# Performance work log

Measured on AMD Instinct MI355X. Metric: run time of the kernel, lower is better.

## Reference

```python
import jax, jax.numpy as jnp
import numpy as np


def setup_inputs() -> dict:
    key = jax.random.key(0)
    k1, k2, k3, k4 = jax.random.split(key, 4)
    B, D_IN, D, N, A = 32, 2048, 128, 400000, 7
    return {
        "x": jax.random.normal(k1, (B, D_IN), dtype=jnp.float32),
        "W_enc": jax.random.normal(k2, (D_IN, D), dtype=jnp.float32) * 0.02,
        "b_enc": jnp.zeros((D,), dtype=jnp.float32),
        "reps": jax.random.normal(k3, (N, D), dtype=jnp.float32),
        "actions": jax.random.normal(k4, (N, A), dtype=jnp.float32),
        "k": 5,
    }


def reference(x, W_enc, b_enc, reps, actions, k):
    # encoder embed: [B, D]
    batch_rep = x @ W_enc + b_enc
    # euclidean cdist: [B, N]
    sq = (
        jnp.sum(batch_rep * batch_rep, axis=-1, keepdims=True)
        + jnp.sum(reps * reps, axis=-1)[None, :]
        - 2.0 * (batch_rep @ reps.T)
    )
    dists = jnp.sqrt(jnp.maximum(sq, 1e-12))
    # top-k smallest distances
    neg_topk, indices = jax.lax.top_k(-dists, k)  # [B, k]
    top_k_distances = -neg_topk
    # gather actions: [B, k, A]
    top_k_actions = actions[indices]
    # softmax(-distance) weights: [B, k]
    weights = jax.nn.softmax(-top_k_distances, axis=1)
    # weighted average: [B, A]
    pred = jnp.sum(top_k_actions * weights[..., None], axis=1)
    return pred
```

## Files before the change

### kernel.cpp

```cpp
#include <hip/hip_runtime.h>
#include <math.h>

#define BATCH 32
#define DIN   2048
#define DK    128
#define NREPS 400000
#define ACT   7
#define TROWS 64
#define NTILE (NREPS / TROWS)
#define STRIDE 132
#define GDEF  694

typedef __attribute__((ext_vector_type(8))) __bf16 bf16x8;
typedef __attribute__((ext_vector_type(4))) float  f32x4;

static __device__ __forceinline__ __bf16 bits2bf(unsigned short v) {
    union { unsigned short u; __bf16 b; } x; x.u = v; return x.b;
}

__device__ __forceinline__ void topk_insert(float s, int n,
    float& d0, float& d1, float& d2, float& d3, float& d4,
    int& i0, int& i1, int& i2, int& i3, int& i4)
{
    if (s < d4) {
        if (s < d3) {
            d4 = d3; i4 = i3;
            if (s < d2) {
                d3 = d2; i3 = i2;
                if (s < d1) {
                    d2 = d1; i2 = i1;
                    if (s < d0) { d1 = d0; i1 = i0; d0 = s; i0 = n; }
                    else        { d1 = s;  i1 = n; }
                } else { d2 = s; i2 = n; }
            } else { d3 = s; i3 = n; }
        } else { d4 = s; i4 = n; }
    }
}

__global__ __launch_bounds__(256) void encoder_kernel(
    const float* __restrict__ x, const float* __restrict__ W,
    const float* __restrict__ be, float* __restrict__ brept,
    float* __restrict__ brnorm)
{
    __shared__ float xs[DIN];
    __shared__ float part[256];
    __shared__ float vrow[DK];
    const int b = blockIdx.x, t = threadIdx.x;

    const float4* x4 = (const float4*)(x + (size_t)b * DIN);
    float4* xs4 = (float4*)xs;
    xs4[t]       = x4[t];
    xs4[t + 256] = x4[t + 256];
    __syncthreads();

    const int d = t & 127, h = t >> 7;
    const float* Wp = W + (size_t)(h * 1024) * DK + d;
    const float* xp = xs + h * 1024;
    float a0 = 0.f, a1 = 0.f, a2 = 0.f, a3 = 0.f;
    for (int i = 0; i < 1024; i += 4) {
        a0 = fmaf(xp[i],     Wp[(size_t)i * DK],       a0);
        a1 = fmaf(xp[i + 1], Wp[(size_t)(i + 1) * DK], a1);
        a2 = fmaf(xp[i + 2], Wp[(size_t)(i + 2) * DK], a2);
        a3 = fmaf(xp[i + 3], Wp[(size_t)(i + 3) * DK], a3);
    }
    part[t] = (a0 + a1) + (a2 + a3);
    __syncthreads();
    if (t < DK) {
        float v = part[t] + part[t + 128] + be[t];
        brept[t * BATCH + b] = -2.0f * v;
        vrow[t] = v * v;
    }
    __syncthreads();
    if (t == 0) {
        float s = 0.f;
        for (int i = 0; i < DK; i++) s += vrow[i];
        brnorm[b] = s;
    }
}

__global__ __launch_bounds__(256, 2) void dist_topk_kernel(
    const float* __restrict__ reps, const float* __restrict__ brt,
    float* __restrict__ pd, int* __restrict__ pi)
{
    __shared__ float tile[TROWS * STRIDE];
    __shared__ float nrmb[TROWS];
    const int t = threadIdx.x, g = blockIdx.x, G = gridDim.x;
    const int wv = t >> 6, ln = t & 63;
    const int c = ln & 15, quad = ln >> 4;
    const int srow = t >> 2, sq = t & 3;

    bf16x8 Bh[2][4], Bl[2][4];
    #pragma unroll
    for (int nt = 0; nt < 2; nt++)
        #pragma unroll
        for (int ks = 0; ks < 4; ks++) {
            bf16x8 h, l;
            #pragma unroll
            for (int j = 0; j < 8; j++) {
                const float f = brt[(ks * 32 + quad * 8 + j) * BATCH + nt * 16 + c];
                const unsigned u = __float_as_uint(f);
                h[j] = bits2bf((unsigned short)(u >> 16));
                const float lf = f - __uint_as_float(u & 0xFFFF0000u);
                l[j] = bits2bf((unsigned short)(__float_as_uint(lf) >> 16));
            }
            Bh[nt][ks] = h; Bl[nt][ks] = l;
        }

    float tA0 = 3.0e38f, tA1 = 3.0e38f, tA2 = 3.0e38f, tA3 = 3.0e38f, tA4 = 3.0e38f;
    int   jA0 = 0, jA1 = 0, jA2 = 0, jA3 = 0, jA4 = 0;
    float tB0 = 3.0e38f, tB1 = 3.0e38f, tB2 = 3.0e38f, tB3 = 3.0e38f, tB4 = 3.0e38f;
    int   jB0 = 0, jB1 = 0, jB2 = 0, jB3 = 0, jB4 = 0;

    {
        const float4* gs = (const float4*)reps + (size_t)g * 2048 + srow * 32 + sq;
        float4 r[8];
        #pragma unroll
        for (int i = 0; i < 8; i++) r[i] = gs[4 * i];
        float s = 0.f;
        #pragma unroll
        for (int i = 0; i < 8; i++) {
            s = fmaf(r[i].x, r[i].x, s); s = fmaf(r[i].y, r[i].y, s);
            s = fmaf(r[i].z, r[i].z, s); s = fmaf(r[i].w, r[i].w, s);
        }
        s += __shfl_xor(s, 1); s += __shfl_xor(s, 2);
        #pragma unroll
        for (int i = 0; i < 8; i++)
            *(f32x4*)&tile[srow * STRIDE + (sq + 4 * i) * 4] =
                (f32x4){r[i].x, r[i].y, r[i].z, r[i].w};
        if ((t & 3) == 0) nrmb[srow] = s;
    }
    __syncthreads();

    int it = g;
    while (true) {
        const int itn = it + G;
        const bool have = itn < NTILE;
        float4 r[8];
        if (have) {
            const float4* gs = (const float4*)reps + (size_t)itn * 2048 + srow * 32 + sq;
            #pragma unroll
            for (int i = 0; i < 8; i++) r[i] = gs[4 * i];
        }

        f32x4 C0 = {0.f, 0.f, 0.f, 0.f}, C1 = {0.f, 0.f, 0.f, 0.f};
        #pragma unroll
        for (int ks = 0; ks < 4; ks++) {
            const float* ap = &tile[(wv * 16 + c) * STRIDE + ks * 32 + quad * 8];
            const f32x4 a0 = *(const f32x4*)ap;
            const f32x4 a1 = *(const f32x4*)(ap + 4);
            bf16x8 ah, al;
            #pragma unroll
            for (int j = 0; j < 8; j++) {
                const float f = (j < 4) ? a0[j] : a1[j - 4];
                const unsigned u = __float_as_uint(f);
                ah[j] = bits2bf((unsigned short)(u >> 16));
                const float lf = f - __uint_as_float(u & 0xFFFF0000u);
                al[j] = bits2bf((unsigned short)(__float_as_uint(lf) >> 16));
            }
            C0 = __builtin_amdgcn_mfma_f32_16x16x32_bf16(ah, Bh[0][ks], C0, 0, 0, 0);
            C0 = __builtin_amdgcn_mfma_f32_16x16x32_bf16(ah, Bl[0][ks], C0, 0, 0, 0);
            C0 = __builtin_amdgcn_mfma_f32_16x16x32_bf16(al, Bh[0][ks], C0, 0, 0, 0);
            C1 = __builtin_amdgcn_mfma_f32_16x16x32_bf16(ah, Bh[1][ks], C1, 0, 0, 0);
            C1 = __builtin_amdgcn_mfma_f32_16x16x32_bf16(ah, Bl[1][ks], C1, 0, 0, 0);
            C1 = __builtin_amdgcn_mfma_f32_16x16x32_bf16(al, Bh[1][ks], C1, 0, 0, 0);
        }
        {
            const int rowb = wv * 16 + quad * 4;
            const int nb = it * TROWS + rowb;
            #pragma unroll
            for (int reg = 0; reg < 4; reg++) {
                const float nr = nrmb[rowb + reg];
                const float s0 = C0[reg] + nr;
                const float s1 = C1[reg] + nr;
                topk_insert(s0, nb + reg, tA0, tA1, tA2, tA3, tA4, jA0, jA1, jA2, jA3, jA4);
                topk_insert(s1, nb + reg, tB0, tB1, tB2, tB3, tB4, jB0, jB1, jB2, jB3, jB4);
            }
        }
        __syncthreads();
        if (have) {
            float s = 0.f;
            #pragma unroll
            for (int i = 0; i < 8; i++) {
                s = fmaf(r[i].x, r[i].x, s); s = fmaf(r[i].y, r[i].y, s);
                s = fmaf(r[i].z, r[i].z, s); s = fmaf(r[i].w, r[i].w, s);
            }
            s += __shfl_xor(s, 1); s += __shfl_xor(s, 2);
            #pragma unroll
            for (int i = 0; i < 8; i++)
                *(f32x4*)&tile[srow * STRIDE + (sq + 4 * i) * 4] =
                    (f32x4){r[i].x, r[i].y, r[i].z, r[i].w};
            if ((t & 3) == 0) nrmb[srow] = s;
        }
        __syncthreads();
        if (!have) break;
        it = itn;
    }

    float* cD = tile;
    int*   cI = (int*)(tile + 2560);
    {
        const int base0 = ((0 * 16 + c) * 16 + (wv * 4 + quad)) * 5;
        cD[base0]     = tA0; cI[base0]     = jA0;
        cD[base0 + 1] = tA1; cI[base0 + 1] = jA1;
        cD[base0 + 2] = tA2; cI[base0 + 2] = jA2;
        cD[base0 + 3] = tA3; cI[base0 + 3] = jA3;
        cD[base0 + 4] = tA4; cI[base0 + 4] = jA4;
        const int base1 = ((16 + c) * 16 + (wv * 4 + quad)) * 5;
        cD[base1]     = tB0; cI[base1]     = jB0;
        cD[base1 + 1] = tB1; cI[base1 + 1] = jB1;
        cD[base1 + 2] = tB2; cI[base1 + 2] = jB2;
        cD[base1 + 3] = tB3; cI[base1 + 3] = jB3;
        cD[base1 + 4] = tB4; cI[base1 + 4] = jB4;
    }
    __syncthreads();
    if (t < 32) {
        float d0 = 3.0e38f, d1 = 3.0e38f, d2 = 3.0e38f, d3 = 3.0e38f, d4 = 3.0e38f;
        int   i0 = 0, i1 = 0, i2 = 0, i3 = 0, i4 = 0;
        for (int s2 = 0; s2 < 16; s2++) {
            const int base = (t * 16 + s2) * 5;
            #pragma unroll
            for (int e = 0; e < 5; e++)
                topk_insert(cD[base + e], cI[base + e],
                            d0, d1, d2, d3, d4, i0, i1, i2, i3, i4);
        }
        const int ob = (g * BATCH + t) * 5;
        pd[ob] = d0; pd[ob + 1] = d1; pd[ob + 2] = d2; pd[ob + 3] = d3; pd[ob + 4] = d4;
        pi[ob] = i0; pi[ob + 1] = i1; pi[ob + 2] = i2; pi[ob + 3] = i3; pi[ob + 4] = i4;
    }
}

__global__ __launch_bounds__(256) void final_kernel(
    const float* __restrict__ pd, const int* __restrict__ pi,
    const float* __restrict__ brnorm, const float* __restrict__ actions,
    const float* __restrict__ reps, const float* __restrict__ brt,
    float* __restrict__ out, int G)
{
    __shared__ float lD[256 * 5];
    __shared__ int   lI[256 * 5];
    __shared__ float sD[32 * 5];
    __shared__ int   sI[32 * 5];
    __shared__ int   exi[10];
    __shared__ float exq[10];
    const int b = blockIdx.x, t = threadIdx.x;

    float d0 = 3.0e38f, d1 = 3.0e38f, d2 = 3.0e38f, d3 = 3.0e38f, d4 = 3.0e38f;
    int   i0 = 0, i1 = 0, i2 = 0, i3 = 0, i4 = 0;
    for (int g = t; g < G; g += 256) {
        const int base = (g * BATCH + b) * 5;
        #pragma unroll
        for (int e = 0; e < 5; e++)
            topk_insert(pd[base + e], pi[base + e],
                        d0, d1, d2, d3, d4, i0, i1, i2, i3, i4);
    }
    lD[t * 5] = d0; lD[t * 5 + 1] = d1; lD[t * 5 + 2] = d2; lD[t * 5 + 3] = d3; lD[t * 5 + 4] = d4;
    lI[t * 5] = i0; lI[t * 5 + 1] = i1; lI[t * 5 + 2] = i2; lI[t * 5 + 3] = i3; lI[t * 5 + 4] = i4;
    __syncthreads();
    if (t < 32) {
        d0 = d1 = d2 = d3 = d4 = 3.0e38f; i0 = i1 = i2 = i3 = i4 = 0;
        for (int s = 0; s < 8; s++) {
            const int base = (t * 8 + s) * 5;
            #pragma unroll
            for (int e = 0; e < 5; e++)
                topk_insert(lD[base + e], lI[base + e],
                            d0, d1, d2, d3, d4, i0, i1, i2, i3, i4);
        }
        sD[t * 5] = d0; sD[t * 5 + 1] = d1; sD[t * 5 + 2] = d2; sD[t * 5 + 3] = d3; sD[t * 5 + 4] = d4;
        sI[t * 5] = i0; sI[t * 5 + 1] = i1; sI[t * 5 + 2] = i2; sI[t * 5 + 3] = i3; sI[t * 5 + 4] = i4;
    }
    __syncthreads();
    if (t == 0) {
        float dd[10]; int ii[10];
        #pragma unroll
        for (int j = 0; j < 10; j++) { dd[j] = 3.0e38f; ii[j] = 0; }
        for (int s2 = 0; s2 < 160; s2++) {
            const float v = sD[s2]; const int ix = sI[s2];
            if (v < dd[9]) {
                int j = 9;
                while (j > 0 && dd[j - 1] > v) { dd[j] = dd[j - 1]; ii[j] = ii[j - 1]; j--; }
                dd[j] = v; ii[j] = ix;
            }
        }
        #pragma unroll
        for (int j = 0; j < 10; j++) exi[j] = ii[j];
    }
    __syncthreads();
    if (t < 80) {
        const int cand = t >> 3, seg = t & 7;
        const int row = exi[cand];
        const float4* rp = (const float4*)(reps + (size_t)row * DK) + seg * 4;
        float s = 0.f;
        #pragma unroll
        for (int q = 0; q < 4; q++) {
            const float4 v = rp[q];
            const int k0 = seg * 16 + q * 4;
            s += v.x * v.x + brt[(k0 + 0) * BATCH + b] * v.x;
            s += v.y * v.y + brt[(k0 + 1) * BATCH + b] * v.y;
            s += v.z * v.z + brt[(k0 + 2) * BATCH + b] * v.z;
            s += v.w * v.w + brt[(k0 + 3) * BATCH + b] * v.w;
        }
        s += __shfl_xor(s, 1); s += __shfl_xor(s, 2); s += __shfl_xor(s, 4);
        if ((t & 7) == 0) exq[cand] = s;
    }
    __syncthreads();
    if (t == 0) {
        const float bn = brnorm[b];
        float dd[10];
        #pragma unroll
        for (int j = 0; j < 10; j++) dd[j] = sqrtf(fmaxf(exq[j] + bn, 1e-12f));
        float dist5[5]; int idx5[5];
        bool used[10] = {false,false,false,false,false,false,false,false,false,false};
        for (int e = 0; e < 5; e++) {
            int am = -1; float mv = 3.0e38f;
            for (int j = 0; j < 10; j++)
                if (!used[j] && dd[j] < mv) { mv = dd[j]; am = j; }
            used[am] = true; dist5[e] = mv; idx5[e] = exi[am];
        }
        const float dmin = dist5[0];
        float w[5], wsum = 0.f;
        #pragma unroll
        for (int e = 0; e < 5; e++) { w[e] = expf(dmin - dist5[e]); wsum += w[e]; }
        const float inv = 1.0f / wsum;
        for (int a = 0; a < ACT; a++) {
            float o = 0.f;
            #pragma unroll
            for (int e = 0; e < 5; e++)
                o = fmaf(w[e], actions[(size_t)idx5[e] * ACT + a], o);
            out[b * ACT + a] = o * inv;
        }
    }
}

extern "C" void kernel_launch(void* const* d_in, const int* in_sizes, int n_in,
                              void* d_out, int out_size, void* d_ws, size_t ws_size,
                              hipStream_t stream)
{
    (void)in_sizes; (void)n_in; (void)out_size;
    const float* x       = (const float*)d_in[0];
    const float* W       = (const float*)d_in[1];
    const float* be      = (const float*)d_in[2];
    const float* reps    = (const float*)d_in[3];
    const float* actions = (const float*)d_in[4];

    float* ws     = (float*)d_ws;
    float* brept  = ws;
    float* brnorm = ws + 4096;
    float* pd     = ws + 4224;

    int G = GDEF;
    {
        const size_t avail_f = ws_size / 4;
        if (avail_f < 4224 + (size_t)G * 320) {
            long fit = ((long)avail_f - 4224) / 320;
            G = (fit < 1) ? 1 : (int)fit;
            if (G > GDEF) G = GDEF;
        }
    }
    int* pi = (int*)(pd + (size_t)G * BATCH * 5);

    encoder_kernel  <<<32, 256, 0, stream>>>(x, W, be, brept, brnorm);
    dist_topk_kernel<<<G,  256, 0, stream>>>(reps, brept, pd, pi);
    final_kernel    <<<32, 256, 0, stream>>>(pd, pi, brnorm, actions, reps, brept,
                                             (float*)d_out, G);
}
```

Before: 496.1 us.

## Stage bf16 hi/lo split planes in LDS and drop register-held B fragments

Each reps tile is now split into packed bf16 hi and lo planes once, when it is written to LDS, and the MFMA loop reads ready-made bf16x8 fragments instead of converting fp32 per wave. The B operand (the batch embedding) is also precomputed into LDS rather than held in registers, which cuts register pressure so the launch bound can rise from 2 to 3 blocks per SM and the grid from 694 to 768. The register prefetch of the next tile is removed in favour of a simple load, convert, sync, compute loop, so overlap now relies on higher occupancy instead of software pipelining. LDS use per block grows to about 52 KB and B fragments are re-read from LDS every tile.

```diff
diff --git a/kernel.cpp b/kernel.cpp
--- a/kernel.cpp
+++ b/kernel.cpp
@@ -8,14 +8,25 @@
 #define ACT   7
 #define TROWS 64
 #define NTILE (NREPS / TROWS)
-#define STRIDE 132
-#define GDEF  694
+#define GDEF  768
+
+#define AHI_OFF 0
+#define ALO_OFF 17408
+#define BF_OFF  34816
+#define NRM_OFF 52224
+#define LDS_BYTES 52480
 
 typedef __attribute__((ext_vector_type(8))) __bf16 bf16x8;
 typedef __attribute__((ext_vector_type(4))) float  f32x4;
 
-static __device__ __forceinline__ __bf16 bits2bf(unsigned short v) {
-    union { unsigned short u; __bf16 b; } x; x.u = v; return x.b;
+static __device__ __forceinline__ unsigned pack_hi(float a, float b) {
+    return (__float_as_uint(a) >> 16) | (__float_as_uint(b) & 0xffff0000u);
+}
+static __device__ __forceinline__ float hi_f(float a) {
+    return __uint_as_float(__float_as_uint(a) & 0xffff0000u);
+}
+static __device__ __forceinline__ unsigned pack_lo(float a, float b) {
+    return pack_hi(a - hi_f(a), b - hi_f(b));
 }
 
 __device__ __forceinline__ void topk_insert(float s, int n,
@@ -78,91 +89,118 @@
     }
 }
 
-__global__ __launch_bounds__(256, 2) void dist_topk_kernel(
+__global__ __launch_bounds__(256, 3) void dist_topk_kernel(
     const float* __restrict__ reps, const float* __restrict__ brt,
     float* __restrict__ pd, int* __restrict__ pi)
 {
-    __shared__ float tile[TROWS * STRIDE];
-    __shared__ float nrmb[TROWS];
+    __shared__ __align__(16) char smem[LDS_BYTES];
+    float* nrmb = (float*)(smem + NRM_OFF);
+
     const int t = threadIdx.x, g = blockIdx.x, G = gridDim.x;
     const int wv = t >> 6, ln = t & 63;
     const int c = ln & 15, quad = ln >> 4;
     const int srow = t >> 2, sq = t & 3;
 
-    bf16x8 Bh[2][4], Bl[2][4];
-    #pragma unroll
-    for (int nt = 0; nt < 2; nt++)
-        #pragma unroll
-        for (int ks = 0; ks < 4; ks++) {
-            bf16x8 h, l;
-            #pragma unroll
-            for (int j = 0; j < 8; j++) {
-                const float f = brt[(ks * 32 + quad * 8 + j) * BATCH + nt * 16 + c];
-                const unsigned u = __float_as_uint(f);
-                h[j] = bits2bf((unsigned short)(u >> 16));
-                const float lf = f - __uint_as_float(u & 0xFFFF0000u);
-                l[j] = bits2bf((unsigned short)(__float_as_uint(lf) >> 16));
-            }
-            Bh[nt][ks] = h; Bl[nt][ks] = l;
-        }
+    for (int idx = t; idx < 1024; idx += 256) {
+        const int fg = idx >> 6, l = idx & 63;
+        const int qc = l & 15, qq = l >> 4;
+        const int plane = fg >> 3, nt = (fg >> 2) & 1, ks = fg & 3;
+        const float* src = brt + (ks * 32 + qq * 8) * BATCH + nt * 16 + qc;
+        const float v0 = src[0],      v1 = src[32],     v2 = src[64],  v3 = src[96];
+        const float v4 = src[128],    v5 = src[160],    v6 = src[192], v7 = src[224];
+        uint4 P;
+        if (plane == 0) {
+            P.x = pack_hi(v0, v1); P.y = pack_hi(v2, v3);
+            P.z = pack_hi(v4, v5); P.w = pack_hi(v6, v7);
+        } else {
+            P.x = pack_lo(v0, v1); P.y = pack_lo(v2, v3);
+            P.z = pack_lo(v4, v5); P.w = pack_lo(v6, v7);
+        }
+        *(uint4*)(smem + BF_OFF + fg * 1088 + qq * 272 + qc * 16) = P;
+    }
 
     float tA0 = 3.0e38f, tA1 = 3.0e38f, tA2 = 3.0e38f, tA3 = 3.0e38f, tA4 = 3.0e38f;
     int   jA0 = 0, jA1 = 0, jA2 = 0, jA3 = 0, jA4 = 0;
     float tB0 = 3.0e38f, tB1 = 3.0e38f, tB2 = 3.0e38f, tB3 = 3.0e38f, tB4 = 3.0e38f;
     int   jB0 = 0, jB1 = 0, jB2 = 0, jB3 = 0, jB4 = 0;
 
-    {
-        const float4* gs = (const float4*)reps + (size_t)g * 2048 + srow * 32 + sq;
-        float4 r[8];
-        #pragma unroll
-        for (int i = 0; i < 8; i++) r[i] = gs[4 * i];
-        float s = 0.f;
-        #pragma unroll
-        for (int i = 0; i < 8; i++) {
-            s = fmaf(r[i].x, r[i].x, s); s = fmaf(r[i].y, r[i].y, s);
-            s = fmaf(r[i].z, r[i].z, s); s = fmaf(r[i].w, r[i].w, s);
-        }
-        s += __shfl_xor(s, 1); s += __shfl_xor(s, 2);
-        #pragma unroll
-        for (int i = 0; i < 8; i++)
-            *(f32x4*)&tile[srow * STRIDE + (sq + 4 * i) * 4] =
-                (f32x4){r[i].x, r[i].y, r[i].z, r[i].w};
-        if ((t & 3) == 0) nrmb[srow] = s;
-    }
-    __syncthreads();
-
-    int it = g;
-    while (true) {
-        const int itn = it + G;
-        const bool have = itn < NTILE;
-        float4 r[8];
-        if (have) {
-            const float4* gs = (const float4*)reps + (size_t)itn * 2048 + srow * 32 + sq;
-            #pragma unroll
-            for (int i = 0; i < 8; i++) r[i] = gs[4 * i];
-        }
+    char* const Ahi_w = smem + AHI_OFF + srow * 272 + sq * 64;
+    char* const Alo_w = smem + ALO_OFF + srow * 272 + sq * 64;
+    char* const Ahi_r = smem + AHI_OFF + (wv * 16 + c) * 272 + quad * 16;
+    char* const Alo_r = smem + ALO_OFF + (wv * 16 + c) * 272 + quad * 16;
+    char* const B_r   = smem + BF_OFF + quad * 272 + c * 16;
+
+    for (int it = g; it < NTILE; it += G) {
+        {
+            const float4* gs = (const float4*)(reps + (size_t)it * (TROWS * DK)
+                                               + srow * DK + sq * 32);
+            const float4 f0 = gs[0], f1 = gs[1], f2 = gs[2], f3 = gs[3];
+            const float4 f4 = gs[4], f5 = gs[5], f6 = gs[6], f7 = gs[7];
+
+            float s = 0.f;
+            s = fmaf(f0.x, f0.x, s); s = fmaf(f0.y, f0.y, s);
+            s = fmaf(f0.z, f0.z, s); s = fmaf(f0.w, f0.w, s);
+            s = fmaf(f1.x, f1.x, s); s = fmaf(f1.y, f1.y, s);
+            s = fmaf(f1.z, f1.z, s); s = fmaf(f1.w, f1.w, s);
+            s = fmaf(f2.x, f2.x, s); s = fmaf(f2.y, f2.y, s);
+            s = fmaf(f2.z, f2.z, s); s = fmaf(f2.w, f2.w, s);
+            s = fmaf(f3.x, f3.x, s); s = fmaf(f3.y, f3.y, s);
+            s = fmaf(f3.z, f3.z, s); s = fmaf(f3.w, f3.w, s);
+            s = fmaf(f4.x, f4.x, s); s = fmaf(f4.y, f4.y, s);
+            s = fmaf(f4.z, f4.z, s); s = fmaf(f4.w, f4.w, s);
+            s = fmaf(f5.x, f5.x, s); s = fmaf(f5.y, f5.y, s);
+            s = fmaf(f5.z, f5.z, s); s = fmaf(f5.w, f5.w, s);
+            s = fmaf(f6.x, f6.x, s); s = fmaf(f6.y, f6.y, s);
+            s = fmaf(f6.z, f6.z, s); s = fmaf(f6.w, f6.w, s);
+            s = fmaf(f7.x, f7.x, s); s = fmaf(f7.y, f7.y, s);
+            s = fmaf(f7.z, f7.z, s); s = fmaf(f7.w, f7.w, s);
+            s += __shfl_xor(s, 1); s += __shfl_xor(s, 2);
+            if (sq == 0) nrmb[srow] = s;
+
+            uint4 P;
+            P.x = pack_hi(f0.x, f0.y); P.y = pack_hi(f0.z, f0.w);
+            P.z = pack_hi(f1.x, f1.y); P.w = pack_hi(f1.z, f1.w);
+            *(uint4*)(Ahi_w) = P;
+            P.x = pack_hi(f2.x, f2.y); P.y = pack_hi(f2.z, f2.w);
+            P.z = pack_hi(f3.x, f3.y); P.w = pack_hi(f3.z, f3.w);
+            *(uint4*)(Ahi_w + 16) = P;
+            P.x = pack_hi(f4.x, f4.y); P.y = pack_hi(f4.z, f4.w);
+            P.z = pack_hi(f5.x, f5.y); P.w = pack_hi(f5.z, f5.w);
+            *(uint4*)(Ahi_w + 32) = P;
+            P.x = pack_hi(f6.x, f6.y); P.y = pack_hi(f6.z, f6.w);
+            P.z = pack_hi(f7.x, f7.y); P.w = pack_hi(f7.z, f7.w);
+            *(uint4*)(Ahi_w + 48) = P;
+
+            P.x = pack_lo(f0.x, f0.y); P.y = pack_lo(f0.z, f0.w);
+            P.z = pack_lo(f1.x, f1.y); P.w = pack_lo(f1.z, f1.w);
+            *(uint4*)(Alo_w) = P;
+            P.x = pack_lo(f2.x, f2.y); P.y = pack_lo(f2.z, f2.w);
+            P.z = pack_lo(f3.x, f3.y); P.w = pack_lo(f3.z, f3.w);
+            *(uint4*)(Alo_w + 16) = P;
+            P.x = pack_lo(f4.x, f4.y); P.y = pack_lo(f4.z, f4.w);
+            P.z = pack_lo(f5.x, f5.y); P.w = pack_lo(f5.z, f5.w);
+            *(uint4*)(Alo_w + 32) = P;
+            P.x = pack_lo(f6.x, f6.y); P.y = pack_lo(f6.z, f6.w);
+            P.z = pack_lo(f7.x, f7.y); P.w = pack_lo(f7.z, f7.w);
+            *(uint4*)(Alo_w + 48) = P;
+        }
+        __syncthreads();
 
         f32x4 C0 = {0.f, 0.f, 0.f, 0.f}, C1 = {0.f, 0.f, 0.f, 0.f};
         #pragma unroll
         for (int ks = 0; ks < 4; ks++) {
-            const float* ap = &tile[(wv * 16 + c) * STRIDE + ks * 32 + quad * 8];
-            const f32x4 a0 = *(const f32x4*)ap;
-            const f32x4 a1 = *(const f32x4*)(ap + 4);
-            bf16x8 ah, al;
-            #pragma unroll
-            for (int j = 0; j < 8; j++) {
-                const float f = (j < 4) ? a0[j] : a1[j - 4];
-                const unsigned u = __float_as_uint(f);
-                ah[j] = bits2bf((unsigned short)(u >> 16));
-                const float lf = f - __uint_as_float(u & 0xFFFF0000u);
-                al[j] = bits2bf((unsigned short)(__float_as_uint(lf) >> 16));
-            }
-            C0 = __builtin_amdgcn_mfma_f32_16x16x32_bf16(ah, Bh[0][ks], C0, 0, 0, 0);
-            C0 = __builtin_amdgcn_mfma_f32_16x16x32_bf16(ah, Bl[0][ks], C0, 0, 0, 0);
-            C0 = __builtin_amdgcn_mfma_f32_16x16x32_bf16(al, Bh[0][ks], C0, 0, 0, 0);
-            C1 = __builtin_amdgcn_mfma_f32_16x16x32_bf16(ah, Bh[1][ks], C1, 0, 0, 0);
-            C1 = __builtin_amdgcn_mfma_f32_16x16x32_bf16(ah, Bl[1][ks], C1, 0, 0, 0);
-            C1 = __builtin_amdgcn_mfma_f32_16x16x32_bf16(al, Bh[1][ks], C1, 0, 0, 0);
+            const bf16x8 ah  = *(const bf16x8*)(Ahi_r + ks * 64);
+            const bf16x8 al  = *(const bf16x8*)(Alo_r + ks * 64);
+            const bf16x8 bh0 = *(const bf16x8*)(B_r + (ks)      * 1088);
+            const bf16x8 bh1 = *(const bf16x8*)(B_r + (4 + ks)  * 1088);
+            const bf16x8 bl0 = *(const bf16x8*)(B_r + (8 + ks)  * 1088);
+            const bf16x8 bl1 = *(const bf16x8*)(B_r + (12 + ks) * 1088);
+            C0 = __builtin_amdgcn_mfma_f32_16x16x32_bf16(ah, bh0, C0, 0, 0, 0);
+            C0 = __builtin_amdgcn_mfma_f32_16x16x32_bf16(ah, bl0, C0, 0, 0, 0);
+            C0 = __builtin_amdgcn_mfma_f32_16x16x32_bf16(al, bh0, C0, 0, 0, 0);
+            C1 = __builtin_amdgcn_mfma_f32_16x16x32_bf16(ah, bh1, C1, 0, 0, 0);
+            C1 = __builtin_amdgcn_mfma_f32_16x16x32_bf16(ah, bl1, C1, 0, 0, 0);
+            C1 = __builtin_amdgcn_mfma_f32_16x16x32_bf16(al, bh1, C1, 0, 0, 0);
         }
         {
             const int rowb = wv * 16 + quad * 4;
@@ -177,29 +215,12 @@
             }
         }
         __syncthreads();
-        if (have) {
-            float s = 0.f;
-            #pragma unroll
-            for (int i = 0; i < 8; i++) {
-                s = fmaf(r[i].x, r[i].x, s); s = fmaf(r[i].y, r[i].y, s);
-                s = fmaf(r[i].z, r[i].z, s); s = fmaf(r[i].w, r[i].w, s);
-            }
-            s += __shfl_xor(s, 1); s += __shfl_xor(s, 2);
-            #pragma unroll
-            for (int i = 0; i < 8; i++)
-                *(f32x4*)&tile[srow * STRIDE + (sq + 4 * i) * 4] =
-                    (f32x4){r[i].x, r[i].y, r[i].z, r[i].w};
-            if ((t & 3) == 0) nrmb[srow] = s;
-        }
-        __syncthreads();
-        if (!have) break;
-        it = itn;
-    }
-
-    float* cD = tile;
-    int*   cI = (int*)(tile + 2560);
+    }
+
+    float* cD = (float*)smem;
+    int*   cI = (int*)smem + 2560;
     {
-        const int base0 = ((0 * 16 + c) * 16 + (wv * 4 + quad)) * 5;
+        const int base0 = ((c) * 16 + (wv * 4 + quad)) * 5;
         cD[base0]     = tA0; cI[base0]     = jA0;
         cD[base0 + 1] = tA1; cI[base0 + 1] = jA1;
         cD[base0 + 2] = tA2; cI[base0 + 2] = jA2;
```

Result: slower. 509.9 us (+2.8%).

## Switch distance GEMM to single fp16 MFMA with swizzled half-precision LDS tile

Applied to the files above, without the earlier changes.

Replaces the three-pass split-bf16 MFMA emulation of fp32 with one fp16 MFMA per k-step. Rep rows are converted to packed fp16 when stored to a smaller XOR-swizzled LDS tile. It also drops the register prefetch/double-buffer pipeline in favour of a simple load-sync-compute loop, and raises the default grid size and removes the occupancy hint. This cuts MFMA and conversion work and LDS footprint, but lowers distance precision, which could change which top-k neighbours are selected, and it loses the overlap of global loads with compute.

```diff
diff --git a/kernel.cpp b/kernel.cpp
--- a/kernel.cpp
+++ b/kernel.cpp
@@ -8,14 +8,19 @@
 #define ACT   7
 #define TROWS 64
 #define NTILE (NREPS / TROWS)
-#define STRIDE 132
-#define GDEF  694
-
-typedef __attribute__((ext_vector_type(8))) __bf16 bf16x8;
-typedef __attribute__((ext_vector_type(4))) float  f32x4;
-
-static __device__ __forceinline__ __bf16 bits2bf(unsigned short v) {
-    union { unsigned short u; __bf16 b; } x; x.u = v; return x.b;
+#define GDEF  1250
+
+#define NRM_OFF 16384
+#define LDS_BYTES 20736
+
+typedef __fp16   fp16x2_b __attribute__((ext_vector_type(2)));
+typedef _Float16 f16x8 __attribute__((ext_vector_type(8)));
+typedef float    f32x4 __attribute__((ext_vector_type(4)));
+
+static __device__ __forceinline__ unsigned pk(float a, float b) {
+    union { fp16x2_b h; unsigned u; } x;
+    x.h = __builtin_amdgcn_cvt_pkrtz(a, b);
+    return x.u;
 }
 
 __device__ __forceinline__ void topk_insert(float s, int n,
@@ -78,92 +83,76 @@
     }
 }
 
-__global__ __launch_bounds__(256, 2) void dist_topk_kernel(
+__global__ __launch_bounds__(256) void dist_topk_kernel(
     const float* __restrict__ reps, const float* __restrict__ brt,
     float* __restrict__ pd, int* __restrict__ pi)
 {
-    __shared__ float tile[TROWS * STRIDE];
-    __shared__ float nrmb[TROWS];
+    __shared__ __align__(16) char smem[LDS_BYTES];
+    float* nrmb = (float*)(smem + NRM_OFF);
+
     const int t = threadIdx.x, g = blockIdx.x, G = gridDim.x;
     const int wv = t >> 6, ln = t & 63;
-    const int c = ln & 15, quad = ln >> 4;
-    const int srow = t >> 2, sq = t & 3;
-
-    bf16x8 Bh[2][4], Bl[2][4];
-    #pragma unroll
-    for (int nt = 0; nt < 2; nt++)
-        #pragma unroll
-        for (int ks = 0; ks < 4; ks++) {
-            bf16x8 h, l;
-            #pragma unroll
-            for (int j = 0; j < 8; j++) {
-                const float f = brt[(ks * 32 + quad * 8 + j) * BATCH + nt * 16 + c];
-                const unsigned u = __float_as_uint(f);
-                h[j] = bits2bf((unsigned short)(u >> 16));
-                const float lf = f - __uint_as_float(u & 0xFFFF0000u);
-                l[j] = bits2bf((unsigned short)(__float_as_uint(lf) >> 16));
-            }
-            Bh[nt][ks] = h; Bl[nt][ks] = l;
-        }
+    const int m = ln & 15, quad = ln >> 4;
+    const int sr = t >> 2, sq = t & 3, srl = sr & 15;
+
+    f16x8 B00, B01, B02, B03, B10, B11, B12, B13;
+    {
+        const float* bp = brt + (quad * 8) * BATCH + m;
+#define LOADB(dst, nt, ks) { \
+        const float* q_ = bp + (ks) * 32 * BATCH + (nt) * 16; \
+        union { f16x8 v; unsigned u[4]; } x_; \
+        x_.u[0] = pk(q_[0],   q_[32]); \
+        x_.u[1] = pk(q_[64],  q_[96]); \
+        x_.u[2] = pk(q_[128], q_[160]); \
+        x_.u[3] = pk(q_[192], q_[224]); \
+        dst = x_.v; }
+        LOADB(B00, 0, 0) LOADB(B01, 0, 1) LOADB(B02, 0, 2) LOADB(B03, 0, 3)
+        LOADB(B10, 1, 0) LOADB(B11, 1, 1) LOADB(B12, 1, 2) LOADB(B13, 1, 3)
+#undef LOADB
+    }
 
     float tA0 = 3.0e38f, tA1 = 3.0e38f, tA2 = 3.0e38f, tA3 = 3.0e38f, tA4 = 3.0e38f;
     int   jA0 = 0, jA1 = 0, jA2 = 0, jA3 = 0, jA4 = 0;
     float tB0 = 3.0e38f, tB1 = 3.0e38f, tB2 = 3.0e38f, tB3 = 3.0e38f, tB4 = 3.0e38f;
     int   jB0 = 0, jB1 = 0, jB2 = 0, jB3 = 0, jB4 = 0;
 
-    {
-        const float4* gs = (const float4*)reps + (size_t)g * 2048 + srow * 32 + sq;
-        float4 r[8];
-        #pragma unroll
-        for (int i = 0; i < 8; i++) r[i] = gs[4 * i];
-        float s = 0.f;
-        #pragma unroll
-        for (int i = 0; i < 8; i++) {
-            s = fmaf(r[i].x, r[i].x, s); s = fmaf(r[i].y, r[i].y, s);
-            s = fmaf(r[i].z, r[i].z, s); s = fmaf(r[i].w, r[i].w, s);
-        }
-        s += __shfl_xor(s, 1); s += __shfl_xor(s, 2);
-        #pragma unroll
-        for (int i = 0; i < 8; i++)
-            *(f32x4*)&tile[srow * STRIDE + (sq + 4 * i) * 4] =
-                (f32x4){r[i].x, r[i].y, r[i].z, r[i].w};
-        if ((t & 3) == 0) nrmb[srow] = s;
-    }
-    __syncthreads();
-
-    int it = g;
-    while (true) {
-        const int itn = it + G;
-        const bool have = itn < NTILE;
-        float4 r[8];
-        if (have) {
-            const float4* gs = (const float4*)reps + (size_t)itn * 2048 + srow * 32 + sq;
-            #pragma unroll
-            for (int i = 0; i < 8; i++) r[i] = gs[4 * i];
-        }
+    const int arow = wv * 16 + m;
+
+    for (int it = g; it < NTILE; it += G) {
+        {
+            const float4* gs = (const float4*)(reps + (size_t)it * (TROWS * DK))
+                               + sr * 32 + sq * 8;
+            float s = 0.f;
+            #pragma unroll 1
+            for (int p = 0; p < 4; p++) {
+                const float4 fa = gs[2 * p];
+                const float4 fb = gs[2 * p + 1];
+                s = fmaf(fa.x, fa.x, s); s = fmaf(fa.y, fa.y, s);
+                s = fmaf(fa.z, fa.z, s); s = fmaf(fa.w, fa.w, s);
+                s = fmaf(fb.x, fb.x, s); s = fmaf(fb.y, fb.y, s);
+                s = fmaf(fb.z, fb.z, s); s = fmaf(fb.w, fb.w, s);
+                uint4 P;
+                P.x = pk(fa.x, fa.y); P.y = pk(fa.z, fa.w);
+                P.z = pk(fb.x, fb.y); P.w = pk(fb.z, fb.w);
+                const int chunk = sq * 4 + p;
+                *(uint4*)(smem + sr * 256 + ((chunk ^ srl) << 4)) = P;
+            }
+            s += __shfl_xor(s, 1); s += __shfl_xor(s, 2);
+            if (sq == 0) nrmb[sr] = s;
+        }
+        __syncthreads();
 
         f32x4 C0 = {0.f, 0.f, 0.f, 0.f}, C1 = {0.f, 0.f, 0.f, 0.f};
-        #pragma unroll
-        for (int ks = 0; ks < 4; ks++) {
-            const float* ap = &tile[(wv * 16 + c) * STRIDE + ks * 32 + quad * 8];
-            const f32x4 a0 = *(const f32x4*)ap;
-            const f32x4 a1 = *(const f32x4*)(ap + 4);
-            bf16x8 ah, al;
-            #pragma unroll
-            for (int j = 0; j < 8; j++) {
-                const float f = (j < 4) ? a0[j] : a1[j - 4];
-                const unsigned u = __float_as_uint(f);
-                ah[j] = bits2bf((unsigned short)(u >> 16));
-                const float lf = f - __uint_as_float(u & 0xFFFF0000u);
-                al[j] = bits2bf((unsigned short)(__float_as_uint(lf) >> 16));
-            }
-            C0 = __builtin_amdgcn_mfma_f32_16x16x32_bf16(ah, Bh[0][ks], C0, 0, 0, 0);
-            C0 = __builtin_amdgcn_mfma_f32_16x16x32_bf16(ah, Bl[0][ks], C0, 0, 0, 0);
-            C0 = __builtin_amdgcn_mfma_f32_16x16x32_bf16(al, Bh[0][ks], C0, 0, 0, 0);
-            C1 = __builtin_amdgcn_mfma_f32_16x16x32_bf16(ah, Bh[1][ks], C1, 0, 0, 0);
-            C1 = __builtin_amdgcn_mfma_f32_16x16x32_bf16(ah, Bl[1][ks], C1, 0, 0, 0);
-            C1 = __builtin_amdgcn_mfma_f32_16x16x32_bf16(al, Bh[1][ks], C1, 0, 0, 0);
-        }
+#define KSTEP(ks, Bn0, Bn1) { \
+        const f16x8 av = *(const f16x8*)(smem + arow * 256 + ((((ks) * 4 + quad) ^ m) << 4)); \
+        C0 = __builtin_amdgcn_mfma_f32_16x16x32_f16(av, Bn0, C0, 0, 0, 0); \
+        C1 = __builtin_amdgcn_mfma_f32_16x16x32_f16(av, Bn1, C1, 0, 0, 0); }
+        KSTEP(0, B00, B10)
+        KSTEP(1, B01, B11)
+        KSTEP(2, B02, B12)
+        KSTEP(3, B03, B13)
+#undef KSTEP
+
         {
             const int rowb = wv * 16 + quad * 4;
             const int nb = it * TROWS + rowb;
@@ -177,35 +166,18 @@
             }
         }
         __syncthreads();
-        if (have) {
-            float s = 0.f;
-            #pragma unroll
-            for (int i = 0; i < 8; i++) {
-                s = fmaf(r[i].x, r[i].x, s); s = fmaf(r[i].y, r[i].y, s);
-                s = fmaf(r[i].z, r[i].z, s); s = fmaf(r[i].w, r[i].w, s);
-            }
-            s += __shfl_xor(s, 1); s += __shfl_xor(s, 2);
-            #pragma unroll
-            for (int i = 0; i < 8; i++)
-                *(f32x4*)&tile[srow * STRIDE + (sq + 4 * i) * 4] =
-                    (f32x4){r[i].x, r[i].y, r[i].z, r[i].w};
-            if ((t & 3) == 0) nrmb[srow] = s;
-        }
-        __syncthreads();
-        if (!have) break;
-        it = itn;
-    }
-
-    float* cD = tile;
-    int*   cI = (int*)(tile + 2560);
+    }
+
+    float* cD = (float*)smem;
+    int*   cI = (int*)smem + 2560;
     {
-        const int base0 = ((0 * 16 + c) * 16 + (wv * 4 + quad)) * 5;
+        const int base0 = (m * 16 + (wv * 4 + quad)) * 5;
         cD[base0]     = tA0; cI[base0]     = jA0;
         cD[base0 + 1] = tA1; cI[base0 + 1] = jA1;
         cD[base0 + 2] = tA2; cI[base0 + 2] = jA2;
         cD[base0 + 3] = tA3; cI[base0 + 3] = jA3;
         cD[base0 + 4] = tA4; cI[base0 + 4] = jA4;
-        const int base1 = ((16 + c) * 16 + (wv * 4 + quad)) * 5;
+        const int base1 = ((16 + m) * 16 + (wv * 4 + quad)) * 5;
         cD[base1]     = tB0; cI[base1]     = jB0;
         cD[base1 + 1] = tB1; cI[base1 + 1] = jB1;
         cD[base1 + 2] = tB2; cI[base1 + 2] = jB2;
```

New measurement: 550.3 us. 10.9% more time.
